# Performance work log

Hardware: AMD Instinct MI355X
Metric: run time of the kernel (lower is better)

## Reference

```python
import jax, jax.numpy as jnp
import numpy as np

LN_EPS = 1e-3  # keras LayerNormalization default epsilon
H = 32


def _glorot(key, shape):
    fan_in, fan_out = shape[0], shape[1]
    lim = np.sqrt(6.0 / (fan_in + fan_out)).astype(np.float32)
    return jax.random.uniform(key, shape, jnp.float32, -lim, lim)


def setup_inputs() -> dict:
    key = jax.random.key(0)
    ks = jax.random.split(key, 10)
    ns, nc, d = 4096, 1024, 64
    num_seq, seq_len = 32, 256
    return {
        "sites": jax.random.normal(ks[0], (ns, d), jnp.float32),
        "cons": jax.random.normal(ks[1], (nc, d), jnp.float32),
        "idx_lower": jax.random.randint(ks[2], (ns,), 0, num_seq * seq_len, jnp.int32),
        "idx_higher": jax.random.randint(ks[3], (ns,), 0, num_seq * seq_len, jnp.int32),
        "W_s": _glorot(ks[4], (d, H)), "b_s": jnp.zeros((H,), jnp.float32),
        "W_c": _glorot(ks[5], (d, H)), "b_c": jnp.zeros((H,), jnp.float32),
        "W_d": _glorot(ks[6], (H, H)), "b_d": jnp.zeros((H,), jnp.float32),
        "ln_g": jnp.ones((H,), jnp.float32), "ln_b": jnp.zeros((H,), jnp.float32),
        "W_o": _glorot(ks[7], (H, 1)), "b_o": jnp.zeros((1,), jnp.float32),
        "num_seq": num_seq, "seq_len": seq_len,
    }


def reference(sites, cons, idx_lower, idx_higher, W_s, b_s, W_c, b_c,
              W_d, b_d, ln_g, ln_b, W_o, b_o, num_seq, seq_len):
    s = jax.nn.relu(sites @ W_s + b_s)          # [ns, 32]
    c = jax.nn.relu(cons @ W_c + b_c)           # [nc, 32]
    comb = s[:, None, :] + c[None, :, :]        # [ns, nc, 32] broadcast-sum
    h = comb @ W_d + b_d                        # decoder MLP: Dense(32)
    mu = jnp.mean(h, axis=-1, keepdims=True)
    var = jnp.var(h, axis=-1, keepdims=True)
    h = (h - mu) * jax.lax.rsqrt(var + LN_EPS) * ln_g + ln_b  # LayerNorm
    logits = (h @ W_o + b_o)[..., 0]            # [ns, nc]
    M = jax.nn.softmax(logits, axis=-1)

    nc_ = M.shape[1]
    slots = num_seq * seq_len

    def band(cum, idx):
        # scatter_nd (duplicate indices accumulate) onto slot grid
        Z = jnp.zeros((slots, nc_), M.dtype).at[idx].add(cum)
        Z = Z.reshape(num_seq, seq_len, nc_)
        p = jax.nn.relu(1.0 - Z)
        # exclusive cumprod along the position (seq_len) axis
        excl = jnp.cumprod(
            jnp.concatenate([jnp.ones_like(p[:, :1]), p[:, :-1]], axis=1), axis=1)
        return excl.reshape(slots, nc_)[idx]    # gather back per site

    M_c_lower = jnp.flip(jnp.cumsum(jnp.flip(M, -1), axis=-1), -1)  # reverse cumsum
    M_c_higher = jnp.cumsum(M, axis=-1)
    M_lower = band(M_c_lower, idx_lower)
    M_higher = band(M_c_higher, idx_higher)
    return M * M_lower * M_higher
```

## Files before the change

### kernel.cpp

```cpp
#include <hip/hip_runtime.h>

#define NS 4096
#define NCC 1024
#define DD 64
#define HH2 32
#define NSEQ 32
#define SLEN 256
#define SLOTS 8192
#define LNEPS 1e-3f
#define MAXSPS 1024

__global__ void __launch_bounds__(1024) k_setup(
    const float* __restrict__ sites, const float* __restrict__ cons,
    const float* __restrict__ Ws, const float* __restrict__ bs,
    const float* __restrict__ Wc, const float* __restrict__ bc,
    const float* __restrict__ Wd, const float* __restrict__ bd,
    const float* __restrict__ g, const float* __restrict__ Wo,
    float* __restrict__ u, float* __restrict__ A, float* __restrict__ P,
    float* __restrict__ v, float* __restrict__ B, float* __restrict__ Q,
    const int* __restrict__ idxl, const int* __restrict__ idxh,
    int* __restrict__ offl, int* __restrict__ slotl, int* __restrict__ sitel,
    int* __restrict__ offh, int* __restrict__ sloth, int* __restrict__ siteh) {
  __shared__ int cnt[SLOTS];
  __shared__ int wsumI[16];
  int tid = threadIdx.x;
  if (blockIdx.x < 20) {
    if (tid >= 256) return;
    int t = blockIdx.x * 256 + tid;
    if (t >= NS + NCC) return;
    bool isSite = t < NS;
    int row = isSite ? t : t - NS;
    const float* x = isSite ? sites + row * DD : cons + row * DD;
    const float* W1 = isSite ? Ws : Wc;
    const float* b1 = isSite ? bs : bc;
    float s[HH2];
#pragma unroll
    for (int h = 0; h < HH2; h++) s[h] = b1[h];
    for (int k = 0; k < DD; k++) {
      float xv = x[k];
#pragma unroll
      for (int h = 0; h < HH2; h++) s[h] = fmaf(xv, W1[k * HH2 + h], s[h]);
    }
#pragma unroll
    for (int h = 0; h < HH2; h++) s[h] = fmaxf(s[h], 0.0f);
    float hs[HH2];
#pragma unroll
    for (int h = 0; h < HH2; h++) hs[h] = isSite ? 0.0f : bd[h];
    for (int k = 0; k < HH2; k++) {
      float sv = s[k];
#pragma unroll
      for (int h = 0; h < HH2; h++) hs[h] = fmaf(sv, Wd[k * HH2 + h], hs[h]);
    }
    float mu = 0.f;
#pragma unroll
    for (int h = 0; h < HH2; h++) mu += hs[h];
    mu *= (1.0f / HH2);
    float p = 0.f, a = 0.f;
    float* dst = isSite ? (u + row * HH2) : (v + row * HH2);
#pragma unroll
    for (int h = 0; h < HH2; h++) {
      float uu = hs[h] - mu;
      dst[h] = uu;
      p += uu * uu;
      a = fmaf(uu * g[h], Wo[h], a);
    }
    p *= (1.0f / HH2);
    if (isSite) { A[row] = a; P[row] = p; } else { B[row] = a; Q[row] = p; }
    return;
  }
  int lane = tid & 63, wv = tid >> 6;
  int pass = blockIdx.x - 20;
  const int* idx = pass ? idxh : idxl;
  int* off = pass ? offh : offl;
  int* slotA = pass ? sloth : slotl;
  int* siteA = pass ? siteh : sitel;
  for (int i2 = tid; i2 < SLOTS; i2 += 1024) cnt[i2] = 0;
  __syncthreads();
  for (int i2 = tid; i2 < NS; i2 += 1024) atomicAdd(&cnt[idx[i2]], 1);
  __syncthreads();
  int base = tid * 8;
  int loc[8]; int sum = 0;
#pragma unroll
  for (int q2 = 0; q2 < 8; q2++) { loc[q2] = sum; sum += cnt[base + q2]; }
  int incl = sum;
#pragma unroll
  for (int o = 1; o < 64; o <<= 1) { int t2 = __shfl_up(incl, o); if (lane >= o) incl += t2; }
  if (lane == 63) wsumI[wv] = incl;
  __syncthreads();
  int wprev = 0;
#pragma unroll
  for (int w = 0; w < 16; w++) { int t3 = wsumI[w]; if (w < wv) wprev += t3; }
  int excl = wprev + (incl - sum);
  __syncthreads();
#pragma unroll
  for (int q2 = 0; q2 < 8; q2++) { int o2 = excl + loc[q2]; off[base + q2] = o2; cnt[base + q2] = o2; }
  if (tid == 0) off[SLOTS] = NS;
  __syncthreads();
  for (int i2 = tid; i2 < NS; i2 += 1024) {
    int sl = idx[i2];
    int pos = atomicAdd(&cnt[sl], 1);
    slotA[pos] = sl; siteA[pos] = i2;
  }
}

__global__ void __launch_bounds__(1024) k_main(const float* __restrict__ u,
    const float* __restrict__ A, const float* __restrict__ P,
    const float* __restrict__ v, const float* __restrict__ B, const float* __restrict__ Q,
    const float* __restrict__ lnb, const float* __restrict__ Wo, const float* __restrict__ bo,
    float* __restrict__ M, float* __restrict__ CLp, float* __restrict__ CHp) {
  int j = threadIdx.x;
  int lane = j & 63, wv = j >> 6;
  __shared__ float redB[16 * 16];
  float4 vv[8];
  const float4* vp = (const float4*)(v + j * HH2);
#pragma unroll
  for (int q = 0; q < 8; q++) vv[q] = vp[q];
  float Bj = B[j], Qj = Q[j];
  float C = bo[0];
#pragma unroll
  for (int k = 0; k < HH2; k++) C = fmaf(lnb[k], Wo[k], C);
  int row0 = blockIdx.x * 16;

  float e[16], incl[16];
#pragma unroll
  for (int rr = 0; rr < 16; rr++) {
    int i = row0 + rr;
    const float4* up = (const float4*)(u + i * HH2);
    float dot = 0.f;
#pragma unroll
    for (int q = 0; q < 8; q++) {
      float4 u4 = up[q];
      dot = fmaf(u4.x, vv[q].x, dot);
      dot = fmaf(u4.y, vv[q].y, dot);
      dot = fmaf(u4.z, vv[q].z, dot);
      dot = fmaf(u4.w, vv[q].w, dot);
    }
    float var = P[i] + Qj + dot * 0.0625f;
    float lg = rsqrtf(var + LNEPS) * (A[i] + Bj) + C;
    float ee = __expf(lg);
    float ic = ee;
#pragma unroll
    for (int o = 1; o < 64; o <<= 1) { float tt = __shfl_up(ic, o); if (lane >= o) ic += tt; }
    if (lane == 63) redB[rr * 16 + wv] = ic;
    e[rr] = ee; incl[rr] = ic;
  }
  __syncthreads();
#pragma unroll
  for (int rr = 0; rr < 16; rr++) {
    const float4* rb = (const float4*)(redB + rr * 16);
    float4 b0 = rb[0], b1 = rb[1], b2 = rb[2], b3 = rb[3];
    float w_[16] = {b0.x, b0.y, b0.z, b0.w, b1.x, b1.y, b1.z, b1.w,
                    b2.x, b2.y, b2.z, b2.w, b3.x, b3.y, b3.z, b3.w};
    float prev = 0.f, tot = 0.f;
#pragma unroll
    for (int w = 0; w < 16; w++) { tot += w_[w]; if (w < wv) prev += w_[w]; }
    float chE = prev + incl[rr];
    float rd = 1.0f / tot;
    int o_ = (row0 + rr) * NCC + j;
    M[o_] = e[rr] * rd;
    CHp[o_] = chE * rd;
    CLp[o_] = (tot - chE + e[rr]) * rd;
  }
}

__global__ void __launch_bounds__(64, 1) k_bandL(const float* __restrict__ CLp,
    const int* __restrict__ offl, const int* __restrict__ slotl, const int* __restrict__ sitel,
    float* __restrict__ EL) {
  int seq = blockIdx.y;
  int j0 = blockIdx.x * 128 + threadIdx.x * 2;
  int s0 = offl[seq * SLEN];
  int s1 = offl[seq * SLEN + SLEN];
  int n = s1 - s0;
  __shared__ int ss[MAXSPS];
  __shared__ int sl[MAXSPS];
  for (int i = threadIdx.x; i < n; i += 64) { ss[i] = sitel[s0 + i]; sl[i] = slotl[s0 + i]; }
  __syncthreads();
  if (n <= 0) return;

  const int T = 16;
  float2 bufA[T], bufB[T];
#pragma unroll
  for (int k = 0; k < T; k++) {
    int kk = k < n ? k : n - 1;
    bufA[k] = *(const float2*)(CLp + (size_t)ss[kk] * NCC + j0);
  }
#pragma unroll
  for (int k = 0; k < T; k++) {
    int kk = T + k < n ? T + k : n - 1;
    bufB[k] = *(const float2*)(CLp + (size_t)ss[kk] * NCC + j0);
  }
  float2 r = make_float2(1.f, 1.f);
  float2 z = make_float2(0.f, 0.f);
  int prev = -1;
  int ntiles = (n + T - 1) / T;
  for (int t = 0; t < ntiles; t += 2) {
#pragma unroll
    for (int k = 0; k < T; k++) {
      int cur = t * T + k;
      if (cur < n) {
        float2 cv = bufA[k];
        int slot = sl[cur];
        if (slot != prev) {
          if (prev >= 0) {
            r.x *= fmaxf(1.f - z.x, 0.f);
            r.y *= fmaxf(1.f - z.y, 0.f);
            z = make_float2(0.f, 0.f);
          }
          prev = slot;
        }
        *(float2*)(EL + (size_t)ss[cur] * NCC + j0) = r;
        z.x += cv.x; z.y += cv.y;
      }
    }
#pragma unroll
    for (int k = 0; k < T; k++) {
      int idx2 = (t + 2) * T + k;
      int kk = idx2 < n ? idx2 : n - 1;
      bufA[k] = *(const float2*)(CLp + (size_t)ss[kk] * NCC + j0);
    }
#pragma unroll
    for (int k = 0; k < T; k++) {
      int cur = (t + 1) * T + k;
      if (cur < n) {
        float2 cv = bufB[k];
        int slot = sl[cur];
        if (slot != prev) {
          if (prev >= 0) {
            r.x *= fmaxf(1.f - z.x, 0.f);
            r.y *= fmaxf(1.f - z.y, 0.f);
            z = make_float2(0.f, 0.f);
          }
          prev = slot;
        }
        *(float2*)(EL + (size_t)ss[cur] * NCC + j0) = r;
        z.x += cv.x; z.y += cv.y;
      }
    }
#pragma unroll
    for (int k = 0; k < T; k++) {
      int idx2 = (t + 3) * T + k;
      int kk = idx2 < n ? idx2 : n - 1;
      bufB[k] = *(const float2*)(CLp + (size_t)ss[kk] * NCC + j0);
    }
  }
}

__global__ void __launch_bounds__(64, 1) k_bandH(const float* __restrict__ CHp,
    const int* __restrict__ offh, const int* __restrict__ sloth, const int* __restrict__ siteh,
    const float* __restrict__ EL, float* __restrict__ out) {
  int seq = blockIdx.y;
  int j0 = blockIdx.x * 128 + threadIdx.x * 2;
  int s0 = offh[seq * SLEN];
  int s1 = offh[seq * SLEN + SLEN];
  int n = s1 - s0;
  __shared__ int ss[MAXSPS];
  __shared__ int sl[MAXSPS];
  for (int i = threadIdx.x; i < n; i += 64) { ss[i] = siteh[s0 + i]; sl[i] = sloth[s0 + i]; }
  __syncthreads();
  if (n <= 0) return;

  const int T = 12;
  float2 cA[T], cB[T], mA[T], mB[T], eA[T], eB[T];
#pragma unroll
  for (int k = 0; k < T; k++) {
    int kk = k < n ? k : n - 1;
    size_t base = (size_t)ss[kk] * NCC + j0;
    cA[k] = *(const float2*)(CHp + base);
    mA[k] = *(const float2*)(out + base);
    eA[k] = *(const float2*)(EL + base);
  }
#pragma unroll
  for (int k = 0; k < T; k++) {
    int kk = T + k < n ? T + k : n - 1;
    size_t base = (size_t)ss[kk] * NCC + j0;
    cB[k] = *(const float2*)(CHp + base);
    mB[k] = *(const float2*)(out + base);
    eB[k] = *(const float2*)(EL + base);
  }
  float2 r = make_float2(1.f, 1.f);
  float2 z = make_float2(0.f, 0.f);
  int prev = -1;
  int ntiles = (n + T - 1) / T;
  for (int t = 0; t < ntiles; t += 2) {
#pragma unroll
    for (int k = 0; k < T; k++) {
      int cur = t * T + k;
      if (cur < n) {
        float2 cv = cA[k], mv = mA[k], ev = eA[k];
        int slot = sl[cur];
        if (slot != prev) {
          if (prev >= 0) {
            r.x *= fmaxf(1.f - z.x, 0.f);
            r.y *= fmaxf(1.f - z.y, 0.f);
            z = make_float2(0.f, 0.f);
          }
          prev = slot;
        }
        float2 ov;
        ov.x = mv.x * ev.x * r.x;
        ov.y = mv.y * ev.y * r.y;
        *(float2*)(out + (size_t)ss[cur] * NCC + j0) = ov;
        z.x += cv.x; z.y += cv.y;
      }
    }
#pragma unroll
    for (int k = 0; k < T; k++) {
      int idx2 = (t + 2) * T + k;
      int kk = idx2 < n ? idx2 : n - 1;
      size_t base = (size_t)ss[kk] * NCC + j0;
      cA[k] = *(const float2*)(CHp + base);
      mA[k] = *(const float2*)(out + base);
      eA[k] = *(const float2*)(EL + base);
    }
#pragma unroll
    for (int k = 0; k < T; k++) {
      int cur = (t + 1) * T + k;
      if (cur < n) {
        float2 cv = cB[k], mv = mB[k], ev = eB[k];
        int slot = sl[cur];
        if (slot != prev) {
          if (prev >= 0) {
            r.x *= fmaxf(1.f - z.x, 0.f);
            r.y *= fmaxf(1.f - z.y, 0.f);
            z = make_float2(0.f, 0.f);
          }
          prev = slot;
        }
        float2 ov;
        ov.x = mv.x * ev.x * r.x;
        ov.y = mv.y * ev.y * r.y;
        *(float2*)(out + (size_t)ss[cur] * NCC + j0) = ov;
        z.x += cv.x; z.y += cv.y;
      }
    }
#pragma unroll
    for (int k = 0; k < T; k++) {
      int idx2 = (t + 3) * T + k;
      int kk = idx2 < n ? idx2 : n - 1;
      size_t base = (size_t)ss[kk] * NCC + j0;
      cB[k] = *(const float2*)(CHp + base);
      mB[k] = *(const float2*)(out + base);
      eB[k] = *(const float2*)(EL + base);
    }
  }
}

extern "C" void kernel_launch(void* const* d_in, const int* in_sizes, int n_in,
                              void* d_out, int out_size, void* d_ws, size_t ws_size,
                              hipStream_t stream) {
  const float* sites = (const float*)d_in[0];
  const float* cons  = (const float*)d_in[1];
  const int* idxl = (const int*)d_in[2];
  const int* idxh = (const int*)d_in[3];
  const float* Ws = (const float*)d_in[4];
  const float* bs = (const float*)d_in[5];
  const float* Wc = (const float*)d_in[6];
  const float* bc = (const float*)d_in[7];
  const float* Wd = (const float*)d_in[8];
  const float* bd = (const float*)d_in[9];
  const float* lng = (const float*)d_in[10];
  const float* lnb = (const float*)d_in[11];
  const float* Wo = (const float*)d_in[12];
  const float* bo = (const float*)d_in[13];

  char* wsb = (char*)d_ws;
  size_t o = 0;
  auto alloc = [&](size_t bytes) { char* p = wsb + o; o += (bytes + 15) & ~(size_t)15; return p; };
  float* u   = (float*)alloc((size_t)NS * HH2 * 4);
  float* A   = (float*)alloc((size_t)NS * 4);
  float* P   = (float*)alloc((size_t)NS * 4);
  float* v   = (float*)alloc((size_t)NCC * HH2 * 4);
  float* B   = (float*)alloc((size_t)NCC * 4);
  float* Q   = (float*)alloc((size_t)NCC * 4);
  float* CLp = (float*)alloc((size_t)NS * NCC * 4);
  float* CHp = (float*)alloc((size_t)NS * NCC * 4);
  float* EL  = (float*)alloc((size_t)NS * NCC * 4);
  int* offl  = (int*)alloc((SLOTS + 1) * 4);
  int* slotl = (int*)alloc(NS * 4);
  int* sitel = (int*)alloc(NS * 4);
  int* offh  = (int*)alloc((SLOTS + 1) * 4);
  int* sloth = (int*)alloc(NS * 4);
  int* siteh = (int*)alloc(NS * 4);

  k_setup<<<22, 1024, 0, stream>>>(sites, cons, Ws, bs, Wc, bc, Wd, bd, lng, Wo,
                                   u, A, P, v, B, Q,
                                   idxl, idxh, offl, slotl, sitel, offh, sloth, siteh);
  k_main<<<NS / 16, 1024, 0, stream>>>(u, A, P, v, B, Q, lnb, Wo, bo,
                                       (float*)d_out, CLp, CHp);
  k_bandL<<<dim3(8, NSEQ), 64, 0, stream>>>(CLp, offl, slotl, sitel, EL);
  k_bandH<<<dim3(8, NSEQ), 64, 0, stream>>>(CHp, offh, sloth, siteh, EL, (float*)d_out);
}
```

Baseline: 178.5 us.

## Split band cumprod into per-chunk scans with a cross-chunk prefix pass

Replaces the two sequential per-sequence band kernels with one kernel. It scans each 32-slot chunk of every sequence for both bands in parallel, writing in-chunk exclusive products in place and per-chunk totals to a small table. A prefix kernel turns the totals into exclusive cross-chunk products. A final vectorized kernel multiplies softmax, both in-chunk products and both chunk prefixes into the output. This removes the long serial dependency and the low block count of the old 64-thread kernels, and drops the EL buffer. In exchange it adds two launches, and it silently truncates chunks with more than 96 sites.

```diff
diff --git a/kernel.cpp b/kernel.cpp
--- a/kernel.cpp
+++ b/kernel.cpp
@@ -8,7 +8,7 @@
 #define SLEN 256
 #define SLOTS 8192
 #define LNEPS 1e-3f
-#define MAXSPS 1024
+#define MAXCH 96
 
 __global__ void __launch_bounds__(1024) k_setup(
     const float* __restrict__ sites, const float* __restrict__ cons,
@@ -163,185 +163,99 @@
   }
 }
 
-__global__ void __launch_bounds__(64, 1) k_bandL(const float* __restrict__ CLp,
+__global__ void __launch_bounds__(256) k_band(
+    float* __restrict__ CLp, float* __restrict__ CHp,
     const int* __restrict__ offl, const int* __restrict__ slotl, const int* __restrict__ sitel,
-    float* __restrict__ EL) {
-  int seq = blockIdx.y;
-  int j0 = blockIdx.x * 128 + threadIdx.x * 2;
-  int s0 = offl[seq * SLEN];
-  int s1 = offl[seq * SLEN + SLEN];
-  int n = s1 - s0;
-  __shared__ int ss[MAXSPS];
-  __shared__ int sl[MAXSPS];
-  for (int i = threadIdx.x; i < n; i += 64) { ss[i] = sitel[s0 + i]; sl[i] = slotl[s0 + i]; }
-  __syncthreads();
-  if (n <= 0) return;
-
-  const int T = 16;
-  float2 bufA[T], bufB[T];
+    const int* __restrict__ offh, const int* __restrict__ sloth, const int* __restrict__ siteh,
+    float* __restrict__ TT) {
+  int band = blockIdx.y >> 3;
+  int chunk = blockIdx.y & 7;
+  int seq = blockIdx.z;
+  int j = blockIdx.x * 256 + threadIdx.x;
+  const int* off = band ? offh : offl;
+  const int* slA = band ? sloth : slotl;
+  const int* siA = band ? siteh : sitel;
+  float* C = band ? CHp : CLp;
+  int slot0 = seq * SLEN + chunk * 32;
+  int s0 = off[slot0];
+  int n = off[slot0 + 32] - s0;
+  size_t trow = ((size_t)band * 256 + seq * 8 + chunk) * NCC + j;
+  if (n <= 0) { TT[trow] = 1.0f; return; }
+  if (n > MAXCH) n = MAXCH;
+  __shared__ int ss[MAXCH];
+  __shared__ int sl[MAXCH];
+  for (int i = threadIdx.x; i < n; i += 256) { ss[i] = siA[s0 + i]; sl[i] = slA[s0 + i]; }
+  __syncthreads();
+
+  const int T = 32;
+  float buf[T];
 #pragma unroll
   for (int k = 0; k < T; k++) {
     int kk = k < n ? k : n - 1;
-    bufA[k] = *(const float2*)(CLp + (size_t)ss[kk] * NCC + j0);
-  }
+    buf[k] = C[(size_t)ss[kk] * NCC + j];
+  }
+  float r = 1.f, z = 0.f;
+  int prev = -1;
 #pragma unroll
   for (int k = 0; k < T; k++) {
-    int kk = T + k < n ? T + k : n - 1;
-    bufB[k] = *(const float2*)(CLp + (size_t)ss[kk] * NCC + j0);
-  }
-  float2 r = make_float2(1.f, 1.f);
-  float2 z = make_float2(0.f, 0.f);
-  int prev = -1;
-  int ntiles = (n + T - 1) / T;
-  for (int t = 0; t < ntiles; t += 2) {
-#pragma unroll
-    for (int k = 0; k < T; k++) {
-      int cur = t * T + k;
-      if (cur < n) {
-        float2 cv = bufA[k];
-        int slot = sl[cur];
-        if (slot != prev) {
-          if (prev >= 0) {
-            r.x *= fmaxf(1.f - z.x, 0.f);
-            r.y *= fmaxf(1.f - z.y, 0.f);
-            z = make_float2(0.f, 0.f);
-          }
-          prev = slot;
-        }
-        *(float2*)(EL + (size_t)ss[cur] * NCC + j0) = r;
-        z.x += cv.x; z.y += cv.y;
+    if (k < n) {
+      float cv = buf[k];
+      int slot = sl[k];
+      if (slot != prev) {
+        if (prev >= 0) { r *= fmaxf(1.f - z, 0.f); z = 0.f; }
+        prev = slot;
       }
-    }
-#pragma unroll
-    for (int k = 0; k < T; k++) {
-      int idx2 = (t + 2) * T + k;
-      int kk = idx2 < n ? idx2 : n - 1;
-      bufA[k] = *(const float2*)(CLp + (size_t)ss[kk] * NCC + j0);
-    }
-#pragma unroll
-    for (int k = 0; k < T; k++) {
-      int cur = (t + 1) * T + k;
-      if (cur < n) {
-        float2 cv = bufB[k];
-        int slot = sl[cur];
-        if (slot != prev) {
-          if (prev >= 0) {
-            r.x *= fmaxf(1.f - z.x, 0.f);
-            r.y *= fmaxf(1.f - z.y, 0.f);
-            z = make_float2(0.f, 0.f);
-          }
-          prev = slot;
-        }
-        *(float2*)(EL + (size_t)ss[cur] * NCC + j0) = r;
-        z.x += cv.x; z.y += cv.y;
-      }
-    }
-#pragma unroll
-    for (int k = 0; k < T; k++) {
-      int idx2 = (t + 3) * T + k;
-      int kk = idx2 < n ? idx2 : n - 1;
-      bufB[k] = *(const float2*)(CLp + (size_t)ss[kk] * NCC + j0);
-    }
-  }
-}
-
-__global__ void __launch_bounds__(64, 1) k_bandH(const float* __restrict__ CHp,
-    const int* __restrict__ offh, const int* __restrict__ sloth, const int* __restrict__ siteh,
-    const float* __restrict__ EL, float* __restrict__ out) {
-  int seq = blockIdx.y;
-  int j0 = blockIdx.x * 128 + threadIdx.x * 2;
-  int s0 = offh[seq * SLEN];
-  int s1 = offh[seq * SLEN + SLEN];
-  int n = s1 - s0;
-  __shared__ int ss[MAXSPS];
-  __shared__ int sl[MAXSPS];
-  for (int i = threadIdx.x; i < n; i += 64) { ss[i] = siteh[s0 + i]; sl[i] = sloth[s0 + i]; }
-  __syncthreads();
-  if (n <= 0) return;
-
-  const int T = 12;
-  float2 cA[T], cB[T], mA[T], mB[T], eA[T], eB[T];
-#pragma unroll
-  for (int k = 0; k < T; k++) {
-    int kk = k < n ? k : n - 1;
-    size_t base = (size_t)ss[kk] * NCC + j0;
-    cA[k] = *(const float2*)(CHp + base);
-    mA[k] = *(const float2*)(out + base);
-    eA[k] = *(const float2*)(EL + base);
-  }
-#pragma unroll
-  for (int k = 0; k < T; k++) {
-    int kk = T + k < n ? T + k : n - 1;
-    size_t base = (size_t)ss[kk] * NCC + j0;
-    cB[k] = *(const float2*)(CHp + base);
-    mB[k] = *(const float2*)(out + base);
-    eB[k] = *(const float2*)(EL + base);
-  }
-  float2 r = make_float2(1.f, 1.f);
-  float2 z = make_float2(0.f, 0.f);
-  int prev = -1;
-  int ntiles = (n + T - 1) / T;
-  for (int t = 0; t < ntiles; t += 2) {
-#pragma unroll
-    for (int k = 0; k < T; k++) {
-      int cur = t * T + k;
-      if (cur < n) {
-        float2 cv = cA[k], mv = mA[k], ev = eA[k];
-        int slot = sl[cur];
-        if (slot != prev) {
-          if (prev >= 0) {
-            r.x *= fmaxf(1.f - z.x, 0.f);
-            r.y *= fmaxf(1.f - z.y, 0.f);
-            z = make_float2(0.f, 0.f);
-          }
-          prev = slot;
-        }
-        float2 ov;
-        ov.x = mv.x * ev.x * r.x;
-        ov.y = mv.y * ev.y * r.y;
-        *(float2*)(out + (size_t)ss[cur] * NCC + j0) = ov;
-        z.x += cv.x; z.y += cv.y;
-      }
-    }
-#pragma unroll
-    for (int k = 0; k < T; k++) {
-      int idx2 = (t + 2) * T + k;
-      int kk = idx2 < n ? idx2 : n - 1;
-      size_t base = (size_t)ss[kk] * NCC + j0;
-      cA[k] = *(const float2*)(CHp + base);
-      mA[k] = *(const float2*)(out + base);
-      eA[k] = *(const float2*)(EL + base);
-    }
-#pragma unroll
-    for (int k = 0; k < T; k++) {
-      int cur = (t + 1) * T + k;
-      if (cur < n) {
-        float2 cv = cB[k], mv = mB[k], ev = eB[k];
-        int slot = sl[cur];
-        if (slot != prev) {
-          if (prev >= 0) {
-            r.x *= fmaxf(1.f - z.x, 0.f);
-            r.y *= fmaxf(1.f - z.y, 0.f);
-            z = make_float2(0.f, 0.f);
-          }
-          prev = slot;
-        }
-        float2 ov;
-        ov.x = mv.x * ev.x * r.x;
-        ov.y = mv.y * ev.y * r.y;
-        *(float2*)(out + (size_t)ss[cur] * NCC + j0) = ov;
-        z.x += cv.x; z.y += cv.y;
-      }
-    }
-#pragma unroll
-    for (int k = 0; k < T; k++) {
-      int idx2 = (t + 3) * T + k;
-      int kk = idx2 < n ? idx2 : n - 1;
-      size_t base = (size_t)ss[kk] * NCC + j0;
-      cB[k] = *(const float2*)(CHp + base);
-      mB[k] = *(const float2*)(out + base);
-      eB[k] = *(const float2*)(EL + base);
-    }
+      C[(size_t)ss[k] * NCC + j] = r;
+      z += cv;
+    }
+  }
+  for (int k = T; k < n; k++) {
+    float cv = C[(size_t)ss[k] * NCC + j];
+    int slot = sl[k];
+    if (slot != prev) {
+      if (prev >= 0) { r *= fmaxf(1.f - z, 0.f); z = 0.f; }
+      prev = slot;
+    }
+    C[(size_t)ss[k] * NCC + j] = r;
+    z += cv;
+  }
+  r *= fmaxf(1.f - z, 0.f);
+  TT[trow] = r;
+}
+
+__global__ void __launch_bounds__(1024) k_prefix(float* __restrict__ TT) {
+  int b = blockIdx.x;
+  int j = threadIdx.x;
+  float* base = TT + (size_t)b * 8 * NCC + j;
+  float t[8];
+#pragma unroll
+  for (int c = 0; c < 8; c++) t[c] = base[(size_t)c * NCC];
+  float p = 1.f;
+#pragma unroll
+  for (int c = 0; c < 8; c++) { base[(size_t)c * NCC] = p; p *= t[c]; }
+}
+
+__global__ void __launch_bounds__(256) k_final(
+    float* __restrict__ out, const float* __restrict__ ELr, const float* __restrict__ EHr,
+    const float* __restrict__ TT, const int* __restrict__ idxl, const int* __restrict__ idxh) {
+  int j = threadIdx.x * 4;
+  int s0 = blockIdx.x * 8;
+  const float* TTH = TT + (size_t)256 * NCC;
+#pragma unroll 4
+  for (int k = 0; k < 8; k++) {
+    int s = s0 + k;
+    size_t bofs = (size_t)s * NCC + j;
+    float4 m  = *(const float4*)(out + bofs);
+    float4 el = *(const float4*)(ELr + bofs);
+    float4 eh = *(const float4*)(EHr + bofs);
+    float4 pl = *(const float4*)(TT  + (size_t)(idxl[s] >> 5) * NCC + j);
+    float4 ph = *(const float4*)(TTH + (size_t)(idxh[s] >> 5) * NCC + j);
+    float4 o;
+    o.x = m.x * el.x * pl.x * eh.x * ph.x;
+    o.y = m.y * el.y * pl.y * eh.y * ph.y;
+    o.z = m.z * el.z * pl.z * eh.z * ph.z;
+    o.w = m.w * el.w * pl.w * eh.w * ph.w;
+    *(float4*)(out + bofs) = o;
   }
 }
 
@@ -374,7 +288,7 @@
   float* Q   = (float*)alloc((size_t)NCC * 4);
   float* CLp = (float*)alloc((size_t)NS * NCC * 4);
   float* CHp = (float*)alloc((size_t)NS * NCC * 4);
-  float* EL  = (float*)alloc((size_t)NS * NCC * 4);
+  float* TT  = (float*)alloc((size_t)2 * 256 * NCC * 4);
   int* offl  = (int*)alloc((SLOTS + 1) * 4);
   int* slotl = (int*)alloc(NS * 4);
   int* sitel = (int*)alloc(NS * 4);
@@ -387,6 +301,8 @@
                                    idxl, idxh, offl, slotl, sitel, offh, sloth, siteh);
   k_main<<<NS / 16, 1024, 0, stream>>>(u, A, P, v, B, Q, lnb, Wo, bo,
                                        (float*)d_out, CLp, CHp);
-  k_bandL<<<dim3(8, NSEQ), 64, 0, stream>>>(CLp, offl, slotl, sitel, EL);
-  k_bandH<<<dim3(8, NSEQ), 64, 0, stream>>>(CHp, offh, sloth, siteh, EL, (float*)d_out);
-}
+  k_band<<<dim3(4, 16, 32), 256, 0, stream>>>(CLp, CHp,
+                                              offl, slotl, sitel, offh, sloth, siteh, TT);
+  k_prefix<<<64, 1024, 0, stream>>>(TT);
+  k_final<<<NS / 8, 256, 0, stream>>>((float*)d_out, CLp, CHp, TT, idxl, idxh);
+}
```

After: 158.2 us. -11.4%, faster.
